# Performance work log

Measured on AMD Instinct MI355X. Metric: run time of the kernel, lower is better.

## Reference

```python
import jax, jax.numpy as jnp
import numpy as np

B, N, S, D, H = 32, 16384, 8, 64, 128  # batch, num_inputs, num_slots, slot_size(==input_size), mlp_hidden
ITERS = 3
EPS = 1e-8
LN_EPS = 1e-5


def _ln(x, g, b):
    m = jnp.mean(x, axis=-1, keepdims=True)
    v = jnp.mean((x - m) ** 2, axis=-1, keepdims=True)
    return (x - m) * jax.lax.rsqrt(v + LN_EPS) * g + b


def setup_inputs() -> dict:
    key = jax.random.key(0)
    ks = jax.random.split(key, 20)
    s = 0.02
    return {
        "x": jax.random.normal(ks[0], (B, N, D), jnp.float32),
        "slot_noise": jax.random.normal(ks[1], (B, S, D), jnp.float32),
        "slots_mu": jax.random.normal(ks[2], (1, S, D), jnp.float32),
        "slots_log_sigma": jax.random.normal(ks[3], (1, S, D), jnp.float32) * 0.1,
        "ln_in_g": jnp.ones((D,), jnp.float32), "ln_in_b": jnp.zeros((D,), jnp.float32),
        "ln_slot_g": jnp.ones((D,), jnp.float32), "ln_slot_b": jnp.zeros((D,), jnp.float32),
        "ln_mlp_g": jnp.ones((D,), jnp.float32), "ln_mlp_b": jnp.zeros((D,), jnp.float32),
        "Wq": jax.random.normal(ks[4], (D, D), jnp.float32) * s,
        "Wk": jax.random.normal(ks[5], (D, D), jnp.float32) * s,
        "Wv": jax.random.normal(ks[6], (D, D), jnp.float32) * s,
        "W_ih": jax.random.normal(ks[7], (3 * D, D), jnp.float32) * s,
        "W_hh": jax.random.normal(ks[8], (3 * D, D), jnp.float32) * s,
        "b_ih": jnp.zeros((3 * D,), jnp.float32),
        "b_hh": jnp.zeros((3 * D,), jnp.float32),
        "W1": jax.random.normal(ks[9], (H, D), jnp.float32) * s,
        "b1": jnp.zeros((H,), jnp.float32),
        "W2": jax.random.normal(ks[10], (D, H), jnp.float32) * s,
        "b2": jnp.zeros((D,), jnp.float32),
    }


def reference(x, slot_noise, slots_mu, slots_log_sigma,
              ln_in_g, ln_in_b, ln_slot_g, ln_slot_b, ln_mlp_g, ln_mlp_b,
              Wq, Wk, Wv, W_ih, W_hh, b_ih, b_hh, W1, b1, W2, b2):
    inputs = _ln(x, ln_in_g, ln_in_b)                      # [B,N,D]
    keys = inputs @ Wk.T                                   # [B,N,D]
    values = inputs @ Wv.T                                 # [B,N,D]
    slots = slots_mu + jnp.exp(slots_log_sigma) * slot_noise  # [B,S,D]
    scale = D ** (-0.5)
    for _ in range(ITERS):
        slots_prev = slots
        q = (_ln(slots, ln_slot_g, ln_slot_b) @ Wq.T) * scale   # [B,S,D]
        attn = jax.nn.softmax(jnp.einsum('bnd,bsd->bns', keys, q), axis=2) + EPS
        attn = attn / jnp.sum(attn, axis=1, keepdims=True)      # weighted mean over inputs
        updates = jnp.einsum('bns,bnd->bsd', attn, values)      # [B,S,D]
        # GRUCell(update, hidden=slots_prev), torch semantics
        gi = updates @ W_ih.T + b_ih
        gh = slots_prev @ W_hh.T + b_hh
        i_r, i_z, i_n = jnp.split(gi, 3, axis=-1)
        h_r, h_z, h_n = jnp.split(gh, 3, axis=-1)
        r = jax.nn.sigmoid(i_r + h_r)
        z = jax.nn.sigmoid(i_z + h_z)
        n = jnp.tanh(i_n + r * h_n)
        upd = (1.0 - z) * n + z * slots_prev
        # residual MLP (full_skip=False: residual around updates)
        slots = upd + jax.nn.relu(_ln(upd, ln_mlp_g, ln_mlp_b) @ W1.T + b1) @ W2.T + b2
    return slots
```

## Files before the change

kernel.cpp:

```cpp
#include <hip/hip_runtime.h>

#define BB 32
#define NN 16384

typedef __attribute__((ext_vector_type(4))) float f4;
typedef __attribute__((ext_vector_type(8))) short short8;

__device__ __forceinline__ unsigned int f2bf(float f) {
  unsigned int u = __float_as_uint(f);
  return (u + 0x7fffu + ((u >> 16) & 1u)) >> 16;
}
__device__ __forceinline__ short bfs(float f) { return (short)f2bf(f); }

__global__ void __launch_bounds__(256) prep_kernel(
    const float* __restrict__ Wq, const float* __restrict__ Wk,
    const float* __restrict__ W_ih, const float* __restrict__ Wv,
    float* __restrict__ M, float* __restrict__ Wihv)
{
  int id = blockIdx.x * 256 + threadIdx.x;
  if (id < 4096) {
    int e1 = id >> 6, e2 = id & 63;
    float acc = 0.f;
    for (int d = 0; d < 64; ++d) acc += Wq[d * 64 + e1] * Wk[d * 64 + e2];
    M[id] = acc;
  } else {
    int t = (id - 4096) >> 6, e = id & 63;
    float acc = 0.f;
    for (int k = 0; k < 64; ++k) acc += W_ih[t * 64 + k] * Wv[k * 64 + e];
    Wihv[t * 64 + e] = acc;
  }
}

__global__ void __launch_bounds__(64) init_qk_kernel(
    const float* __restrict__ noise, const float* __restrict__ mu,
    const float* __restrict__ lsig, float* __restrict__ slots,
    const float* __restrict__ gs, const float* __restrict__ bsl,
    const float* __restrict__ M, unsigned short* __restrict__ qkb)
{
  const int bsi = blockIdx.x, l = threadIdx.x;
  const int idx = bsi * 64 + l;
  __shared__ float sh[64];
  float v = mu[idx & 511] + __expf(lsig[idx & 511]) * noise[idx];
  slots[idx] = v;
  float sm = v, sq = v * v;
#pragma unroll
  for (int m = 1; m < 64; m <<= 1) { sm += __shfl_xor(sm, m); sq += __shfl_xor(sq, m); }
  float mean = sm * (1.f / 64.f);
  float var = sq * (1.f / 64.f) - mean * mean;
  sh[l] = (v - mean) * rsqrtf(var + 1e-5f) * gs[l] + bsl[l];
  float acc = 0.f;
  for (int k = 0; k < 64; ++k) acc += sh[k] * M[k * 64 + l];
  qkb[idx] = (unsigned short)f2bf(acc * 0.125f);
}

template <int MODE>
__global__ void __launch_bounds__(256) attn_kernel(
    const float* __restrict__ x, const unsigned short* __restrict__ Xin,
    const float* __restrict__ gin, const float* __restrict__ bin,
    unsigned short* __restrict__ Xout,
    const unsigned short* __restrict__ qkb,
    float* __restrict__ Wpart, float* __restrict__ cpart)
{
  __shared__ __align__(16) unsigned short SMEM[16896];

  const int tid = threadIdx.x, wave = tid >> 6, lane = tid & 63;
  const int l15 = lane & 15, quad = lane >> 4;
  const int blk = blockIdx.x;
  const int b = blk >> 5;
  const int k0 = quad * 8;

  unsigned short* xt  = SMEM + wave * 3584;
  unsigned short* Ptw = SMEM + 14336 + wave * 640;

  const unsigned short* qrow = qkb + (((b << 3) + (l15 & 7)) << 6) + k0;
  const short8 qkA0 = *(const short8*)qrow;
  const short8 qkA1 = *(const short8*)(qrow + 32);

  f4 g0a, g0b, g1a, g1b, h0a, h0b, h1a, h1b;
  if constexpr (MODE == 0) {
    g0a = *(const f4*)(gin + k0);      g0b = *(const f4*)(gin + k0 + 4);
    g1a = *(const f4*)(gin + k0 + 32); g1b = *(const f4*)(gin + k0 + 36);
    h0a = *(const f4*)(bin + k0);      h0b = *(const f4*)(bin + k0 + 4);
    h1a = *(const f4*)(bin + k0 + 32); h1b = *(const f4*)(bin + k0 + 36);
  }

  const size_t row00 = (size_t)blk * 512 + wave * 32 + l15;

  f4 wacc[4];
#pragma unroll
  for (int t = 0; t < 4; ++t) wacc[t] = (f4){0.f, 0.f, 0.f, 0.f};
  float cac0 = 0.f, cac1 = 0.f, cac2 = 0.f, cac3 = 0.f;

  f4 cc[2][4];
  short8 aa[2][2];
  if constexpr (MODE == 0) {
    const float* xp = x + row00 * 64 + k0;
#pragma unroll
    for (int s = 0; s < 2; ++s) {
      const float* sp = xp + s * 1024;
      cc[s][0] = *(const f4*)sp;        cc[s][1] = *(const f4*)(sp + 4);
      cc[s][2] = *(const f4*)(sp + 32); cc[s][3] = *(const f4*)(sp + 36);
    }
  } else {
    const unsigned short* xb = Xin + row00 * 64 + k0;
#pragma unroll
    for (int s = 0; s < 2; ++s) {
      aa[s][0] = *(const short8*)(xb + s * 1024);
      aa[s][1] = *(const short8*)(xb + s * 1024 + 32);
    }
  }

#pragma unroll
  for (int u = 0; u < 4; ++u) {
    f4 nc[2][4];
    short8 na[2][2];
    if (u < 3) {
      if constexpr (MODE == 0) {
        const float* xp = x + (row00 + (size_t)(u + 1) * 128) * 64 + k0;
#pragma unroll
        for (int s = 0; s < 2; ++s) {
          const float* sp = xp + s * 1024;
          nc[s][0] = *(const f4*)sp;        nc[s][1] = *(const f4*)(sp + 4);
          nc[s][2] = *(const f4*)(sp + 32); nc[s][3] = *(const f4*)(sp + 36);
        }
      } else {
        const unsigned short* xb = Xin + (row00 + (size_t)(u + 1) * 128) * 64 + k0;
#pragma unroll
        for (int s = 0; s < 2; ++s) {
          na[s][0] = *(const short8*)(xb + s * 1024);
          na[s][1] = *(const short8*)(xb + s * 1024 + 32);
        }
      }
    }

#pragma unroll
    for (int s = 0; s < 2; ++s) {
      short8 a0, a1;
      if constexpr (MODE == 0) {
        float sm = 0.f, sq = 0.f;
#pragma unroll
        for (int j = 0; j < 4; ++j) {
          float v0 = cc[s][0][j], v1 = cc[s][1][j], v2 = cc[s][2][j], v3 = cc[s][3][j];
          sm += v0 + v1 + v2 + v3;
          sq += v0 * v0 + v1 * v1 + v2 * v2 + v3 * v3;
        }
        sm += __shfl_xor(sm, 16); sq += __shfl_xor(sq, 16);
        sm += __shfl_xor(sm, 32); sq += __shfl_xor(sq, 32);
        const float mean = sm * (1.f / 64.f);
        const float var = sq * (1.f / 64.f) - mean * mean;
        const float rstd = rsqrtf(var + 1e-5f);
#pragma unroll
        for (int j = 0; j < 4; ++j) {
          a0[j]     = bfs((cc[s][0][j] - mean) * rstd * g0a[j] + h0a[j]);
          a0[j + 4] = bfs((cc[s][1][j] - mean) * rstd * g0b[j] + h0b[j]);
          a1[j]     = bfs((cc[s][2][j] - mean) * rstd * g1a[j] + h1a[j]);
          a1[j + 4] = bfs((cc[s][3][j] - mean) * rstd * g1b[j] + h1b[j]);
        }
        unsigned short* xo = Xout + (row00 + (size_t)u * 128 + s * 16) * 64 + k0;
        *(short8*)xo = a0;
        *(short8*)(xo + 32) = a1;
      } else {
        a0 = aa[s][0]; a1 = aa[s][1];
      }

      {
        const int nn = s * 16 + l15;
        unsigned short* xb0 = xt + (quad << 3) + nn;
#pragma unroll
        for (int jj = 0; jj < 8; ++jj) {
          xb0[(k0 + jj) * 56]        = (unsigned short)a0[jj];
          xb0[(k0 + jj + 32) * 56]   = (unsigned short)a1[jj];
        }
      }

      f4 lg = (f4){0.f, 0.f, 0.f, 0.f};
      lg = __builtin_amdgcn_mfma_f32_16x16x32_bf16(qkA0, a0, lg, 0, 0, 0);
      lg = __builtin_amdgcn_mfma_f32_16x16x32_bf16(qkA1, a1, lg, 0, 0, 0);
      const float e0 = __expf(lg[0]), e1 = __expf(lg[1]);
      const float e2 = __expf(lg[2]), e3 = __expf(lg[3]);
      float ss = e0 + e1 + e2 + e3;
      ss += __shfl_xor(ss, 16);
      ss += __shfl_xor(ss, 32);
      const float rs = __builtin_amdgcn_rcpf(ss * 0.5f);
      const float p0 = e0 * rs, p1 = e1 * rs, p2 = e2 * rs, p3 = e3 * rs;
      cac0 += p0; cac1 += p1; cac2 += p2; cac3 += p3;
      unsigned short* pw = Ptw + (quad << 2) * 40 + s * 16 + l15;
      pw[0]   = (unsigned short)f2bf(p0);
      pw[40]  = (unsigned short)f2bf(p1);
      pw[80]  = (unsigned short)f2bf(p2);
      pw[120] = (unsigned short)f2bf(p3);
    }

    short8 pf = *(const short8*)(Ptw + l15 * 40 + quad * 8);
#pragma unroll
    for (int t = 0; t < 4; ++t) {
      const int rr = t * 16 + l15;
      const short8 cvv =
          *(const short8*)(xt + rr * 56 + (((rr >> 3) & 3) << 3) + (quad << 3));
      wacc[t] = __builtin_amdgcn_mfma_f32_16x16x32_bf16(pf, cvv, wacc[t], 0, 0, 0);
    }

    if (u < 3) {
      if constexpr (MODE == 0) {
#pragma unroll
        for (int s = 0; s < 2; ++s)
#pragma unroll
          for (int j = 0; j < 4; ++j) cc[s][j] = nc[s][j];
      } else {
#pragma unroll
        for (int s = 0; s < 2; ++s) { aa[s][0] = na[s][0]; aa[s][1] = na[s][1]; }
      }
    }
  }

#pragma unroll
  for (int m = 1; m < 16; m <<= 1) {
    cac0 += __shfl_xor(cac0, m); cac1 += __shfl_xor(cac1, m);
    cac2 += __shfl_xor(cac2, m); cac3 += __shfl_xor(cac3, m);
  }
  float* redw  = (float*)(SMEM + wave * 3584);
  float* credw = (float*)(SMEM + wave * 3584 + 1024);
  if (l15 == 0 && quad < 2) {
    credw[quad * 4 + 0] = cac0; credw[quad * 4 + 1] = cac1;
    credw[quad * 4 + 2] = cac2; credw[quad * 4 + 3] = cac3;
  }
  if (quad < 2) {
#pragma unroll
    for (int t = 0; t < 4; ++t)
#pragma unroll
      for (int r = 0; r < 4; ++r)
        redw[(quad * 4 + r) * 64 + (t << 4) + l15] = wacc[t][r];
  }
  __syncthreads();
  for (int i = tid; i < 512; i += 256) {
    float acc = 0.f;
#pragma unroll
    for (int w = 0; w < 4; ++w) acc += ((const float*)(SMEM + w * 3584))[i];
    Wpart[(size_t)blk * 512 + i] = acc;
  }
  if (tid < 8) {
    float acc = 0.f;
#pragma unroll
    for (int w = 0; w < 4; ++w) acc += ((const float*)(SMEM + w * 3584 + 1024))[tid];
    cpart[blk * 8 + tid] = acc;
  }
}

__global__ void __launch_bounds__(256) update_kernel(
    const float* __restrict__ Wpart, const float* __restrict__ cpart,
    const float* __restrict__ slots, float* __restrict__ out,
    const float* __restrict__ Wihv, const float* __restrict__ W_hh,
    const float* __restrict__ b_ih, const float* __restrict__ b_hh,
    const float* __restrict__ g_mlp, const float* __restrict__ b_mlp,
    const float* __restrict__ W1, const float* __restrict__ b1,
    const float* __restrict__ W2, const float* __restrict__ b2,
    const float* __restrict__ gs, const float* __restrict__ bsl,
    const float* __restrict__ M, unsigned short* __restrict__ qkb, int make_q)
{
  const int bs = blockIdx.x;
  const int b = bs >> 3, s = bs & 7;
  const int tid = threadIdx.x;
  const int l = tid & 63, cq = tid >> 6;
  __shared__ float wred[4][64];
  __shared__ float credS[4];
  __shared__ float u_sh[64], sp_sh[64], giA[192], ghA[192], uln_sh[64], h_sh[128];

  float wp = 0.f, cp2 = 0.f;
  for (int c = cq * 8; c < cq * 8 + 8; ++c) {
    wp += Wpart[(size_t)(((b << 5) + c) * 8 + s) * 64 + l];
    cp2 += cpart[((b << 5) + c) * 8 + s];
  }
  wred[cq][l] = wp;
  if (l == 0) credS[cq] = cp2;
  __syncthreads();

  float sp = 0.f;
  if (tid < 64) {
    const float cs = credS[0] + credS[1] + credS[2] + credS[3];
    const float u = (wred[0][l] + wred[1][l] + wred[2][l] + wred[3][l]) / cs;
    sp = slots[(b * 8 + s) * 64 + l];
    u_sh[l] = u; sp_sh[l] = sp;
  }
  __syncthreads();

  if (tid < 192) {
    float accI = b_ih[tid], accH = b_hh[tid];
    const float* wi = Wihv + tid * 64;
    const float* wh = W_hh + tid * 64;
    for (int k = 0; k < 64; ++k) { accI += u_sh[k] * wi[k]; accH += sp_sh[k] * wh[k]; }
    giA[tid] = accI; ghA[tid] = accH;
  }
  __syncthreads();

  float upd = 0.f;
  if (tid < 64) {
    const float rg = 1.f / (1.f + __expf(-(giA[l] + ghA[l])));
    const float zg = 1.f / (1.f + __expf(-(giA[64 + l] + ghA[64 + l])));
    const float ng = tanhf(giA[128 + l] + rg * ghA[128 + l]);
    upd = (1.f - zg) * ng + zg * sp;
    float sm = upd, sq = upd * upd;
#pragma unroll
    for (int m = 1; m < 64; m <<= 1) { sm += __shfl_xor(sm, m); sq += __shfl_xor(sq, m); }
    const float mean = sm * (1.f / 64.f);
    const float var = sq * (1.f / 64.f) - mean * mean;
    uln_sh[l] = (upd - mean) * rsqrtf(var + 1e-5f) * g_mlp[l] + b_mlp[l];
  }
  __syncthreads();

  if (tid < 128) {
    float acc = b1[tid];
    const float* w1 = W1 + tid * 64;
    for (int k = 0; k < 64; ++k) acc += uln_sh[k] * w1[k];
    h_sh[tid] = fmaxf(acc, 0.f);
  }
  __syncthreads();

  if (tid < 64) {
    float acc = b2[l];
    const float* w2 = W2 + l * 128;
    for (int k = 0; k < 128; ++k) acc += h_sh[k] * w2[k];
    const float sv = upd + acc;
    out[(b * 8 + s) * 64 + l] = sv;
    if (make_q) {
      float sm2 = sv, sq2 = sv * sv;
#pragma unroll
      for (int m = 1; m < 64; m <<= 1) { sm2 += __shfl_xor(sm2, m); sq2 += __shfl_xor(sq2, m); }
      const float mean2 = sm2 * (1.f / 64.f);
      const float var2 = sq2 * (1.f / 64.f) - mean2 * mean2;
      u_sh[l] = (sv - mean2) * rsqrtf(var2 + 1e-5f) * gs[l] + bsl[l];
      float qa = 0.f;
      for (int k = 0; k < 64; ++k) qa += u_sh[k] * M[k * 64 + l];
      qkb[(b * 8 + s) * 64 + l] = (unsigned short)f2bf(qa * 0.125f);
    }
  }
}

extern "C" void kernel_launch(void* const* d_in, const int* in_sizes, int n_in,
                              void* d_out, int out_size, void* d_ws, size_t ws_size,
                              hipStream_t stream) {
  const float* x       = (const float*)d_in[0];
  const float* noise   = (const float*)d_in[1];
  const float* mu      = (const float*)d_in[2];
  const float* lsig    = (const float*)d_in[3];
  const float* ln_in_g = (const float*)d_in[4];
  const float* ln_in_b = (const float*)d_in[5];
  const float* ln_sl_g = (const float*)d_in[6];
  const float* ln_sl_b = (const float*)d_in[7];
  const float* ln_ml_g = (const float*)d_in[8];
  const float* ln_ml_b = (const float*)d_in[9];
  const float* Wq      = (const float*)d_in[10];
  const float* Wk      = (const float*)d_in[11];
  const float* Wv      = (const float*)d_in[12];
  const float* W_ih    = (const float*)d_in[13];
  const float* W_hh    = (const float*)d_in[14];
  const float* b_ih    = (const float*)d_in[15];
  const float* b_hh    = (const float*)d_in[16];
  const float* W1      = (const float*)d_in[17];
  const float* b1      = (const float*)d_in[18];
  const float* W2      = (const float*)d_in[19];
  const float* b2      = (const float*)d_in[20];

  unsigned short* Xn  = (unsigned short*)d_ws;
  unsigned short* qkb = Xn + (size_t)BB * NN * 64;
  float* M     = (float*)(qkb + 16384);
  float* Wihv  = M + 4096;
  float* slots = Wihv + 12288;
  float* Wpart = slots + 16384;
  float* cpart = Wpart + (size_t)1024 * 512;

  prep_kernel<<<dim3(64), dim3(256), 0, stream>>>(Wq, Wk, W_ih, Wv, M, Wihv);
  init_qk_kernel<<<dim3(256), dim3(64), 0, stream>>>(
      noise, mu, lsig, slots, ln_sl_g, ln_sl_b, M, qkb);

  attn_kernel<0><<<dim3(1024), dim3(256), 0, stream>>>(
      x, nullptr, ln_in_g, ln_in_b, Xn, qkb, Wpart, cpart);

  for (int it = 0; it < 3; ++it) {
    update_kernel<<<dim3(256), dim3(256), 0, stream>>>(
        Wpart, cpart, slots, (it == 2) ? (float*)d_out : slots,
        Wihv, W_hh, b_ih, b_hh, ln_ml_g, ln_ml_b, W1, b1, W2, b2,
        ln_sl_g, ln_sl_b, M, qkb, (it < 2) ? 1 : 0);
    if (it < 2)
      attn_kernel<1><<<dim3(1024), dim3(256), 0, stream>>>(
          x, Xn, ln_in_g, ln_in_b, nullptr, qkb, Wpart, cpart);
  }
}
```

Before: 301.3 us.

## Store transposed normalized inputs so later attention passes skip LDS transpose

The first attention pass now also writes a transposed bf16 copy of the normalized inputs (feature-major) to global memory. Later passes load the MFMA B operand for the weighted sum straight from that copy, which removes the per-iteration LDS transpose writes and reads and shrinks shared memory for those passes. In exchange the first pass does an extra 64 MiB of global writes, later passes read the data twice (row-major and transposed), and the workspace doubles.

Measured after the change: 342.3 us. 1.14x slower.

```diff
diff --git a/kernel.cpp b/kernel.cpp
--- a/kernel.cpp
+++ b/kernel.cpp
@@ -57,11 +57,12 @@
 __global__ void __launch_bounds__(256) attn_kernel(
     const float* __restrict__ x, const unsigned short* __restrict__ Xin,
     const float* __restrict__ gin, const float* __restrict__ bin,
-    unsigned short* __restrict__ Xout,
+    unsigned short* __restrict__ Xout, unsigned short* __restrict__ XnT,
     const unsigned short* __restrict__ qkb,
     float* __restrict__ Wpart, float* __restrict__ cpart)
 {
-  __shared__ __align__(16) unsigned short SMEM[16896];
+  constexpr int SMS = (MODE == 0) ? 16896 : 6720;
+  __shared__ __align__(16) unsigned short SMEM[SMS];
 
   const int tid = threadIdx.x, wave = tid >> 6, lane = tid & 63;
   const int l15 = lane & 15, quad = lane >> 4;
@@ -69,8 +70,9 @@
   const int b = blk >> 5;
   const int k0 = quad * 8;
 
-  unsigned short* xt  = SMEM + wave * 3584;
-  unsigned short* Ptw = SMEM + 14336 + wave * 640;
+  unsigned short* xt  = (MODE == 0) ? (SMEM + wave * 3584) : nullptr;
+  unsigned short* Ptw = (MODE == 0) ? (SMEM + 14336 + wave * 640)
+                                    : (SMEM + wave * 640);
 
   const unsigned short* qrow = qkb + (((b << 3) + (l15 & 7)) << 6) + k0;
   const short8 qkA0 = *(const short8*)qrow;
@@ -85,6 +87,7 @@
   }
 
   const size_t row00 = (size_t)blk * 512 + wave * 32 + l15;
+  const int nbase = ((blk & 31) << 9) + (wave << 5);
 
   f4 wacc[4];
 #pragma unroll
@@ -93,6 +96,11 @@
 
   f4 cc[2][4];
   short8 aa[2][2];
+  short8 cv[4];
+  const unsigned short* vB =
+      (MODE == 1) ? (XnT + (((size_t)((b << 6) + l15)) << 14) + nbase + (quad << 3))
+                  : nullptr;
+
   if constexpr (MODE == 0) {
     const float* xp = x + row00 * 64 + k0;
 #pragma unroll
@@ -108,12 +116,16 @@
       aa[s][0] = *(const short8*)(xb + s * 1024);
       aa[s][1] = *(const short8*)(xb + s * 1024 + 32);
     }
+#pragma unroll
+    for (int t = 0; t < 4; ++t)
+      cv[t] = *(const short8*)(vB + ((size_t)t << 18));
   }
 
 #pragma unroll
   for (int u = 0; u < 4; ++u) {
     f4 nc[2][4];
     short8 na[2][2];
+    short8 nv[4];
     if (u < 3) {
       if constexpr (MODE == 0) {
         const float* xp = x + (row00 + (size_t)(u + 1) * 128) * 64 + k0;
@@ -130,6 +142,9 @@
           na[s][0] = *(const short8*)(xb + s * 1024);
           na[s][1] = *(const short8*)(xb + s * 1024 + 32);
         }
+#pragma unroll
+        for (int t = 0; t < 4; ++t)
+          nv[t] = *(const short8*)(vB + ((size_t)t << 18) + ((u + 1) << 7));
       }
     }
 
@@ -159,18 +174,15 @@
         unsigned short* xo = Xout + (row00 + (size_t)u * 128 + s * 16) * 64 + k0;
         *(short8*)xo = a0;
         *(short8*)(xo + 32) = a1;
+        const int nn = s * 16 + l15;
+        unsigned short* xb0 = xt + (quad << 3) + nn;
+#pragma unroll
+        for (int jj = 0; jj < 8; ++jj) {
+          xb0[(k0 + jj) * 56]      = (unsigned short)a0[jj];
+          xb0[(k0 + jj + 32) * 56] = (unsigned short)a1[jj];
+        }
       } else {
         a0 = aa[s][0]; a1 = aa[s][1];
-      }
-
-      {
-        const int nn = s * 16 + l15;
-        unsigned short* xb0 = xt + (quad << 3) + nn;
-#pragma unroll
-        for (int jj = 0; jj < 8; ++jj) {
-          xb0[(k0 + jj) * 56]        = (unsigned short)a0[jj];
-          xb0[(k0 + jj + 32) * 56]   = (unsigned short)a1[jj];
-        }
       }
 
       f4 lg = (f4){0.f, 0.f, 0.f, 0.f};
@@ -194,10 +206,26 @@
     short8 pf = *(const short8*)(Ptw + l15 * 40 + quad * 8);
 #pragma unroll
     for (int t = 0; t < 4; ++t) {
-      const int rr = t * 16 + l15;
-      const short8 cvv =
-          *(const short8*)(xt + rr * 56 + (((rr >> 3) & 3) << 3) + (quad << 3));
+      short8 cvv;
+      if constexpr (MODE == 0) {
+        const int rr = t * 16 + l15;
+        cvv = *(const short8*)(xt + rr * 56 + (((rr >> 3) & 3) << 3) + (quad << 3));
+      } else {
+        cvv = cv[t];
+      }
       wacc[t] = __builtin_amdgcn_mfma_f32_16x16x32_bf16(pf, cvv, wacc[t], 0, 0, 0);
+    }
+
+    if constexpr (MODE == 0) {
+      const int nb = nbase + (u << 7);
+#pragma unroll
+      for (int pass = 0; pass < 4; ++pass) {
+        const int e = (pass << 4) + (lane >> 2);
+        const int no = (lane & 3) << 3;
+        const short8 vv =
+            *(const short8*)(xt + e * 56 + (((e >> 3) & 3) << 3) + no);
+        *(short8*)(XnT + (((size_t)((b << 6) + e)) << 14) + nb + no) = vv;
+      }
     }
 
     if (u < 3) {
@@ -209,6 +237,8 @@
       } else {
 #pragma unroll
         for (int s = 0; s < 2; ++s) { aa[s][0] = na[s][0]; aa[s][1] = na[s][1]; }
+#pragma unroll
+        for (int t = 0; t < 4; ++t) cv[t] = nv[t];
       }
     }
   }
@@ -218,8 +248,15 @@
     cac0 += __shfl_xor(cac0, m); cac1 += __shfl_xor(cac1, m);
     cac2 += __shfl_xor(cac2, m); cac3 += __shfl_xor(cac3, m);
   }
-  float* redw  = (float*)(SMEM + wave * 3584);
-  float* credw = (float*)(SMEM + wave * 3584 + 1024);
+  float* redw;
+  float* credw;
+  if constexpr (MODE == 0) {
+    redw  = (float*)(SMEM + wave * 3584);
+    credw = (float*)(SMEM + wave * 3584 + 1024);
+  } else {
+    redw  = (float*)(SMEM + 2560) + wave * 512;
+    credw = (float*)(SMEM + 6656) + wave * 8;
+  }
   if (l15 == 0 && quad < 2) {
     credw[quad * 4 + 0] = cac0; credw[quad * 4 + 1] = cac1;
     credw[quad * 4 + 2] = cac2; credw[quad * 4 + 3] = cac3;
@@ -235,13 +272,21 @@
   for (int i = tid; i < 512; i += 256) {
     float acc = 0.f;
 #pragma unroll
-    for (int w = 0; w < 4; ++w) acc += ((const float*)(SMEM + w * 3584))[i];
+    for (int w = 0; w < 4; ++w) {
+      const float* rw = (MODE == 0) ? (const float*)(SMEM + w * 3584)
+                                    : (const float*)(SMEM + 2560) + w * 512;
+      acc += rw[i];
+    }
     Wpart[(size_t)blk * 512 + i] = acc;
   }
   if (tid < 8) {
     float acc = 0.f;
 #pragma unroll
-    for (int w = 0; w < 4; ++w) acc += ((const float*)(SMEM + w * 3584 + 1024))[tid];
+    for (int w = 0; w < 4; ++w) {
+      const float* cw = (MODE == 0) ? (const float*)(SMEM + w * 3584 + 1024)
+                                    : (const float*)(SMEM + 6656) + w * 8;
+      acc += cw[tid];
+    }
     cpart[blk * 8 + tid] = acc;
   }
 }
@@ -361,7 +406,8 @@
   const float* b2      = (const float*)d_in[20];
 
   unsigned short* Xn  = (unsigned short*)d_ws;
-  unsigned short* qkb = Xn + (size_t)BB * NN * 64;
+  unsigned short* XnT = Xn + (size_t)BB * NN * 64;
+  unsigned short* qkb = XnT + (size_t)BB * NN * 64;
   float* M     = (float*)(qkb + 16384);
   float* Wihv  = M + 4096;
   float* slots = Wihv + 12288;
@@ -373,7 +419,7 @@
       noise, mu, lsig, slots, ln_sl_g, ln_sl_b, M, qkb);
 
   attn_kernel<0><<<dim3(1024), dim3(256), 0, stream>>>(
-      x, nullptr, ln_in_g, ln_in_b, Xn, qkb, Wpart, cpart);
+      x, nullptr, ln_in_g, ln_in_b, Xn, XnT, qkb, Wpart, cpart);
 
   for (int it = 0; it < 3; ++it) {
     update_kernel<<<dim3(256), dim3(256), 0, stream>>>(
@@ -382,6 +428,6 @@
         ln_sl_g, ln_sl_b, M, qkb, (it < 2) ? 1 : 0);
     if (it < 2)
       attn_kernel<1><<<dim3(1024), dim3(256), 0, stream>>>(
-          x, Xn, ln_in_g, ln_in_b, nullptr, qkb, Wpart, cpart);
-  }
-}
+          x, Xn, ln_in_g, ln_in_b, nullptr, XnT, qkb, Wpart, cpart);
+  }
+}
```
